# Performance work log

Measured on AMD Instinct MI355X. Metric: run time of the kernel, lower is better.

Reference implementation:

```python
import jax, jax.numpy as jnp
import numpy as np

EPS = 1e-5
K = 20
NH = 16
SLOPE = 0.2

def leaky(x):
    return jnp.where(x >= 0, x, SLOPE * x)

def bn(x, g, b, axes):
    # training-mode batch norm (biased variance), channel axis = 1
    m = x.mean(axes, keepdims=True)
    v = x.var(axes, keepdims=True)
    shp = [1] * x.ndim
    shp[1] = -1
    return (x - m) / jnp.sqrt(v + EPS) * g.reshape(shp) + b.reshape(shp)

def efr(x, idx, w, k):
    # x: [B, C, N]; idx: flat global gather indices [B*N*k]; w: [C_out, 2C+1]
    B, C, N = x.shape
    xt = x.transpose(0, 2, 1).reshape(B * N, C)
    feature = xt[idx].reshape(B, N, k, C)            # gathered neighbors
    xc = xt.reshape(B, N, 1, C)
    fmean = feature.mean(-1, keepdims=True)          # [B,N,k,1]
    f = jnp.concatenate([feature - xc, fmean, jnp.broadcast_to(xc, feature.shape)], axis=3)
    return jnp.einsum('bnkc,oc->bonk', f, w)         # 1x1 conv -> [B,C_out,N,k]


def setup_inputs() -> dict:
    key = jax.random.key(0)
    ks = jax.random.split(key, 24)
    B, N = 8, 4096
    IN_CH, FEAT_CH, OUT_CH = 6, 64, 64
    d = {}
    d['points'] = jax.random.normal(ks[0], (B, IN_CH // 2, N), dtype=jnp.float32)
    d['feat'] = jax.random.normal(ks[1], (B, FEAT_CH // 2, N), dtype=jnp.float32)
    d['idx'] = jax.random.randint(ks[2], (B * N * K,), 0, B * N)
    s = 0.1
    d['w_efr_p'] = jax.random.normal(ks[3], (IN_CH, IN_CH + 1), dtype=jnp.float32) * s
    d['w_efr_f'] = jax.random.normal(ks[4], (FEAT_CH, FEAT_CH + 1), dtype=jnp.float32) * s
    d['w_q'] = jax.random.normal(ks[5], (FEAT_CH, FEAT_CH // 2), dtype=jnp.float32) * s
    d['g_q'] = jnp.ones((FEAT_CH,), jnp.float32)
    d['b_q'] = jnp.zeros((FEAT_CH,), jnp.float32)
    d['w_pos1'] = jax.random.normal(ks[6], (IN_CH, IN_CH // 2), dtype=jnp.float32) * s
    d['g_pos1'] = jnp.ones((IN_CH,), jnp.float32)
    d['b_pos1'] = jnp.zeros((IN_CH,), jnp.float32)
    d['w_pos2'] = jax.random.normal(ks[7], (FEAT_CH, IN_CH), dtype=jnp.float32) * s
    d['w_attn'] = jax.random.normal(ks[8], (NH * IN_CH, FEAT_CH), dtype=jnp.float32) * s
    d['g1'] = jnp.ones((NH,), jnp.float32)
    d['b1'] = jnp.zeros((NH,), jnp.float32)
    d['w_lin'] = jax.random.normal(ks[9], (OUT_CH, NH), dtype=jnp.float32) * s
    d['g_lin'] = jnp.ones((OUT_CH,), jnp.float32)
    d['b_lin'] = jnp.zeros((OUT_CH,), jnp.float32)
    d['w_res'] = jax.random.normal(ks[10], (OUT_CH, FEAT_CH), dtype=jnp.float32) * s
    d['g_res'] = jnp.ones((OUT_CH,), jnp.float32)
    d['b_res'] = jnp.zeros((OUT_CH,), jnp.float32)
    return d


def reference(points, feat, idx, w_efr_p, w_efr_f, w_q, g_q, b_q,
              w_pos1, g_pos1, b_pos1, w_pos2, w_attn, g1, b1,
              w_lin, g_lin, b_lin, w_res, g_res, b_res):
    B, _, N = points.shape
    knn_points = efr(points, idx, w_efr_p, K)   # [B,6,N,K]
    knn_feat = efr(feat, idx, w_efr_f, K)       # [B,64,N,K]
    x_q = leaky(bn(jnp.einsum('bcn,oc->bon', feat, w_q), g_q, b_q, (0, 2)))
    pos = leaky(bn(jnp.einsum('bcn,oc->bon', points, w_pos1), g_pos1, b_pos1, (0, 2)))
    pos = pos[:, :, :, None] - knn_points       # [B,6,N,K]
    pos = jnp.einsum('bcnk,oc->bonk', pos, w_pos2)  # [B,64,N,K]
    attn = x_q[:, :, :, None] - knn_feat + pos
    attn = jax.nn.softmax(attn / float(np.sqrt(knn_feat.shape[1])), axis=-1)
    attn = jnp.einsum('bcnk,oc->bonk', attn, w_attn)  # [B,NH*6,N,K]
    attn5 = attn.transpose(0, 2, 3, 1).reshape(B, N, K, NH, -1)  # [B,N,K,NH,6]
    y = jnp.einsum('bnkhc,bcnk->bhnk', attn5, knn_points)        # [B,NH,N,K]
    y = leaky(bn(y, g1, b1, (0, 2, 3)))
    y = bn(jnp.einsum('bcnk,oc->bonk', y, w_lin), g_lin, b_lin, (0, 2, 3))
    res = bn(jnp.einsum('bcnk,oc->bonk', knn_feat, w_res), g_res, b_res, (0, 2, 3))
    y = leaky(y + res)
    return y.max(axis=-1)                        # [B,64,N]
```

## Files before the change

kernel.cpp:

```cpp
#include <hip/hip_runtime.h>

#define KNN 20
#define NN 4096
#define NPTS 32768
#define PPW 8

using short8 = __attribute__((ext_vector_type(8))) short;
using f32x4v = __attribute__((ext_vector_type(4))) float;
using uint4v = __attribute__((ext_vector_type(4))) unsigned int;

__device__ __forceinline__ float lrelu(float x){ return x >= 0.f ? x : 0.2f*x; }
__device__ __forceinline__ unsigned short f2b(float x){
    union { float f; unsigned u; } v; v.f = x;
    unsigned r = v.u + 0x7FFFu + ((v.u >> 16) & 1u);
    return (unsigned short)(r >> 16);
}
__device__ __forceinline__ float b2f(unsigned h){
    union { unsigned u; float f; } v; v.u = h << 16; return v.f;
}
#define WSYNC() do { asm volatile("s_waitcnt lgkmcnt(0)" ::: "memory"); __builtin_amdgcn_sched_barrier(0); } while(0)

__device__ __forceinline__ int fslot(int fragi, int klocal, int gp){
    return fragi*1024 + (((klocal) + ((gp)<<4)) ^ ((gp)*5))*16;
}

__global__ void kprep(const float* __restrict__ weff, const float* __restrict__ wattn,
                      const float* __restrict__ wres, const float* __restrict__ wl,
                      unsigned short* __restrict__ packW, float* __restrict__ wdiff,
                      float* __restrict__ w32t, float* __restrict__ wrb,
                      float* __restrict__ rww)
{
    __shared__ float sres[4096];
    __shared__ float sweff[4160];
    __shared__ float scomb[2048];
    int t = threadIdx.x;
    for (int m=t; m<4096; m+=256) sres[m] = wres[m];
    for (int m=t; m<4160; m+=256) sweff[m] = weff[m];
    __syncthreads();
    for (int q=t;q<2048;q+=256){
        int c=q>>5, j=q&31;
        wdiff[q] = sweff[c*65+33+j]-sweff[c*65+j];
    }
    if (t<64) w32t[t] = sweff[t*65+32];
    for (int q=t;q<2048;q+=256){
        int o=q>>5, j=q&31;
        float a=0.f, b=0.f;
        for (int c=0;c<64;c++){
            float wr = sres[o*64+c];
            a += wr*sweff[c*65+j];
            b += wr*(sweff[c*65+33+j]-sweff[c*65+j]);
        }
        scomb[q]=a; wrb[q]=b;
    }
    if (t<64){
        float a=0.f;
        for (int c=0;c<64;c++) a += sres[t*64+c]*sweff[c*65+32];
        rww[t]=a;
    }
    __syncthreads();
    for (int q = t; q < 1536; q += 256){
        int f = q >> 6, l = q & 63;
        #pragma unroll
        for (int j=0;j<8;j++){
            int koff, n; float v;
            if (f < 4){ n = f*16 + (l&15); koff = 0;
                int k = koff + (j>=4?16:0) + 4*(l>>4) + (j&3);
                v = sweff[n*65 + k];
            } else if (f < 16){ int ff=f-4; n = (ff>>1)*16 + (l&15); koff = (ff&1)*32;
                int k = koff + (j>=4?16:0) + 4*(l>>4) + (j&3);
                v = wattn[n*64 + k];
            } else { int ff=f-16; n = (ff>>1)*16 + (l&15); koff = (ff&1)*32;
                int k = koff + (j>=4?16:0) + 4*(l>>4) + (j&3);
                v = sres[n*64 + k];
            }
            packW[(size_t)(f*64+l)*8 + j] = f2b(v);
        }
    }
    for (int q=t;q<512;q+=256){
        int f=q>>6, l=q&63;
        int nt = f&3; bool iswl = f>=4;
        #pragma unroll
        for (int j=0;j<8;j++){
            int kdim = (j>=4?16:0)+4*(l>>4)+(j&3);
            float v;
            if (!iswl) v = scomb[(nt*16+(l&15))*32 + kdim];
            else v = (kdim<16) ? wl[(nt*16+(l&15))*16 + kdim] : 0.f;
            packW[(size_t)((24+f)*64+l)*8+j] = f2b(v);
        }
    }
}

__global__ void __launch_bounds__(256) k0_prep(
    const float* __restrict__ pts, const float* __restrict__ feat,
    const float* __restrict__ wq, const float* __restrict__ wpos1,
    const float* __restrict__ wefp, const float* __restrict__ wdiff,
    const float* __restrict__ wrb,
    unsigned short* __restrict__ ft16, float* __restrict__ pt4,
    unsigned short* __restrict__ qp16, float* __restrict__ pp,
    unsigned short* __restrict__ base16, float* __restrict__ bpp,
    unsigned short* __restrict__ rb16,
    float* __restrict__ qsum, float* __restrict__ qsq,
    float* __restrict__ psum, float* __restrict__ psq)
{
    __shared__ float swq[2048];
    __shared__ float swd[2048];
    __shared__ float swr[2048];
    __shared__ float red[4][64], red2[4][64];
    int tid = threadIdx.x;
    for (int m=tid;m<2048;m+=256){ swq[m]=wq[m]; swd[m]=wdiff[m]; swr[m]=wrb[m]; }
    __syncthreads();
    int r = blockIdx.x*256 + tid;
    int b = r >> 12, n = r & 4095;
    float p0 = pts[((size_t)b*3+0)*NN+n];
    float p1 = pts[((size_t)b*3+1)*NN+n];
    float p2 = pts[((size_t)b*3+2)*NN+n];
    float pm = (p0+p1+p2)*(1.f/3.f);
    *(float4*)(pt4 + (size_t)r*4) = make_float4(p0,p1,p2,pm);
    float f[32];
    #pragma unroll
    for (int c=0;c<32;c++) f[c] = feat[((size_t)b*32+c)*NN+n];
    #pragma unroll
    for (int c=0;c<32;c+=2){
        unsigned pk = (unsigned)f2b(f[c]) | ((unsigned)f2b(f[c+1])<<16);
        *(unsigned*)(ft16 + (size_t)r*32 + c) = pk;
    }
    float q[64];
    for (int o=0;o<64;o++){
        float a=0.f;
        #pragma unroll
        for (int c=0;c<32;c++) a += swq[o*32+c]*f[c];
        q[o]=a;
    }
    for (int o=0;o<64;o+=2){
        unsigned pk = (unsigned)f2b(q[o]) | ((unsigned)f2b(q[o+1])<<16);
        *(unsigned*)(qp16 + (size_t)r*64 + o) = pk;
    }
    int lane = tid & 63, wvv = tid>>6;
    for (int o=0;o<64;o++){
        float s=q[o], s2=q[o]*q[o];
        for (int d=1; d<64; d<<=1){ s += __shfl_xor(s,d); s2 += __shfl_xor(s2,d); }
        if (lane==0){ red[wvv][o]=s; red2[wvv][o]=s2; }
    }
    __syncthreads();
    if (tid<64){
        atomicAdd(qsum+tid, red[0][tid]+red[1][tid]+red[2][tid]+red[3][tid]);
        atomicAdd(qsq+tid, red2[0][tid]+red2[1][tid]+red2[2][tid]+red2[3][tid]);
    }
    for (int o=0;o<64;o++){
        float a=0.f;
        #pragma unroll
        for (int c=0;c<32;c++) a += swd[o*32+c]*f[c];
        q[o]=a;
    }
    for (int o=0;o<64;o+=2){
        unsigned pk = (unsigned)f2b(q[o]) | ((unsigned)f2b(q[o+1])<<16);
        *(unsigned*)(base16 + (size_t)r*64 + o) = pk;
    }
    for (int o=0;o<64;o++){
        float a=0.f;
        #pragma unroll
        for (int c=0;c<32;c++) a += swr[o*32+c]*f[c];
        q[o]=a;
    }
    for (int o=0;o<64;o+=2){
        unsigned pk = (unsigned)f2b(q[o]) | ((unsigned)f2b(q[o+1])<<16);
        *(unsigned*)(rb16 + (size_t)r*64 + o) = pk;
    }
    float pr[8];
    #pragma unroll
    for (int o=0;o<6;o++) pr[o] = wpos1[o*3]*p0 + wpos1[o*3+1]*p1 + wpos1[o*3+2]*p2;
    pr[6]=0.f; pr[7]=0.f;
    *(float4*)(pp+(size_t)r*8)   = make_float4(pr[0],pr[1],pr[2],pr[3]);
    *(float4*)(pp+(size_t)r*8+4) = make_float4(pr[4],pr[5],pr[6],pr[7]);
    __syncthreads();
    for (int o=0;o<6;o++){
        float s=pr[o], s2=pr[o]*pr[o];
        for (int d=1;d<64;d<<=1){ s += __shfl_xor(s,d); s2 += __shfl_xor(s2,d); }
        if (lane==0){ red[wvv][o]=s; red2[wvv][o]=s2; }
    }
    __syncthreads();
    if (tid<6){
        atomicAdd(psum+tid, red[0][tid]+red[1][tid]+red[2][tid]+red[3][tid]);
        atomicAdd(psq+tid, red2[0][tid]+red2[1][tid]+red2[2][tid]+red2[3][tid]);
    }
    #pragma unroll
    for (int j=0;j<6;j++)
        bpp[(size_t)r*8+j] = p0*(wefp[j*7+4]-wefp[j*7]) + p1*(wefp[j*7+5]-wefp[j*7+1])
                           + p2*(wefp[j*7+6]-wefp[j*7+2]);
    bpp[(size_t)r*8+6]=0.f; bpp[(size_t)r*8+7]=0.f;
}

__global__ void k1_paramsA(
    const float* __restrict__ qsum, const float* __restrict__ qsq,
    const float* __restrict__ psum, const float* __restrict__ psq,
    const float* __restrict__ gq, const float* __restrict__ bq,
    const float* __restrict__ gp, const float* __restrict__ bp,
    float* __restrict__ bnq_a, float* __restrict__ bnq_c,
    float* __restrict__ bnp_a, float* __restrict__ bnp_c)
{
    int t = threadIdx.x;
    const float inv = 1.f/32768.f;
    if (t < 64){
        float m = qsum[t]*inv; float v = qsq[t]*inv - m*m;
        float a = gq[t]*rsqrtf(v + 1e-5f);
        bnq_a[t] = a; bnq_c[t] = bq[t] - m*a;
    }
    if (t < 6){
        float m = psum[t]*inv; float v = psq[t]*inv - m*m;
        float a = gp[t]*rsqrtf(v + 1e-5f);
        bnp_a[t] = a; bnp_c[t] = bp[t] - m*a;
    }
}

#define ARENA 12544
#define ANB   0
#define ATR   2048
#define KFR   6272
#define SFM   10368
#define SSKP  10496
#define SIDX  11136
#define YST   11776

__global__ void __launch_bounds__(256, 3) k2_main(
    const unsigned short* __restrict__ ft16, const float* __restrict__ pt4,
    const unsigned short* __restrict__ qp16, const float* __restrict__ pp,
    const unsigned short* __restrict__ base16, const float* __restrict__ bpp,
    const int* __restrict__ idx,
    const float* __restrict__ wefp, const float* __restrict__ wpos2,
    const unsigned short* __restrict__ packW, const float* __restrict__ w32t,
    const float* __restrict__ bnq_a, const float* __restrict__ bnq_c,
    const float* __restrict__ bnp_a, const float* __restrict__ bnp_c,
    unsigned short* __restrict__ yv,
    float* __restrict__ yslot, float* __restrict__ rslot)
{
    __shared__ __align__(16) char smem_[4*ARENA];
    const int tid = threadIdx.x;
    const int l = tid & 63, wv = tid >> 6;
    const int lo = l & 15, g = l >> 4;
    char* S = smem_ + wv*ARENA;
    const int srd = (l ^ (g*5))*16;

    float w2r[4][6], w32r[4], bnqa[4], bnqc[4];
    #pragma unroll
    for (int nt=0;nt<4;nt++){
        #pragma unroll
        for (int j=0;j<6;j++) w2r[nt][j] = wpos2[(nt*16+lo)*6+j];
        w32r[nt] = w32t[nt*16+lo];
        bnqa[nt] = bnq_a[nt*16+lo];
        bnqc[nt] = bnq_c[nt*16+lo];
    }
    float bnpa[6], bnpc[6];
    #pragma unroll
    for (int j=0;j<6;j++){ bnpa[j]=bnp_a[j]; bnpc[j]=bnp_c[j]; }

    float ysum=0.f, ysq=0.f;
    float racc[4]={0.f,0.f,0.f,0.f}, rsqa[4]={0.f,0.f,0.f,0.f};

    const int rbase = blockIdx.x*(4*PPW) + wv*PPW;

    *(int*)(S+SIDX+l*4)        = idx[(size_t)rbase*KNN + l];
    *(int*)(S+SIDX+(64+l)*4)   = idx[(size_t)rbase*KNN + 64 + l];
    if (l < 32) *(int*)(S+SIDX+(128+l)*4) = idx[(size_t)rbase*KNN + 128 + l];
    WSYNC();

    uint2 ng0, ng1; uint2 ng2 = make_uint2(0u,0u); float4 ngp4 = make_float4(0,0,0,0);
    unsigned short nqr[4], nbr[4];
    float nppr[6], nbppr[6];
    float xqv[4], basev[4], sp[6];

#define ISSUE(pi_) { \
    int sb = (pi_)*KNN*4; size_t rr = (size_t)(rbase + (pi_)); \
    int i0 = *(const int*)(S+SIDX+sb+(l>>3)*4); \
    int i1 = *(const int*)(S+SIDX+sb+(8+(l>>3))*4); \
    ng0 = *(const uint2*)(ft16 + (size_t)i0*32 + (l&7)*4); \
    ng1 = *(const uint2*)(ft16 + (size_t)i1*32 + (l&7)*4); \
    if (l < 32){ int i2 = *(const int*)(S+SIDX+sb+(16+(l>>3))*4); \
                 ng2 = *(const uint2*)(ft16 + (size_t)i2*32 + (l&7)*4); } \
    if (l < KNN){ int ip = *(const int*)(S+SIDX+sb+l*4); \
                  ngp4 = *(const float4*)(pt4 + (size_t)ip*4); } \
    _Pragma("unroll") for (int nt=0;nt<4;nt++){ \
        nqr[nt] = qp16[rr*64 + nt*16+lo]; nbr[nt] = base16[rr*64 + nt*16+lo]; } \
    _Pragma("unroll") for (int j=0;j<6;j++){ nppr[j] = pp[rr*8+j]; nbppr[j] = bpp[rr*8+j]; } \
    __builtin_amdgcn_sched_barrier(0); \
}

#define STAGE() { \
    float s0 = b2f(ng0.x&0xffffu)+b2f(ng0.x>>16)+b2f(ng0.y&0xffffu)+b2f(ng0.y>>16); \
    float s1 = b2f(ng1.x&0xffffu)+b2f(ng1.x>>16)+b2f(ng1.y&0xffffu)+b2f(ng1.y>>16); \
    float s2 = b2f(ng2.x&0xffffu)+b2f(ng2.x>>16)+b2f(ng2.y&0xffffu)+b2f(ng2.y>>16); \
    s0 += __shfl_xor(s0,1); s0 += __shfl_xor(s0,2); s0 += __shfl_xor(s0,4); \
    s1 += __shfl_xor(s1,1); s1 += __shfl_xor(s1,2); s1 += __shfl_xor(s1,4); \
    s2 += __shfl_xor(s2,1); s2 += __shfl_xor(s2,2); s2 += __shfl_xor(s2,4); \
    if ((l&7)==0){ \
        *(float*)(S+SFM+(l>>3)*4) = s0*(1.f/32.f); \
        *(float*)(S+SFM+(8+(l>>3))*4) = s1*(1.f/32.f); \
        if (l < 32) *(float*)(S+SFM+(16+(l>>3))*4) = s2*(1.f/32.f); \
    } \
    { int kk = l>>3, gp_ = l&3, jb = ((l>>2)&1)*8; \
      *(uint2*)(S + ANB + fslot(0, kk, gp_) + jb) = ng0; \
      *(uint2*)(S + ANB + fslot(0, 8+kk, gp_) + jb) = ng1; \
      if (l < 32) *(uint2*)(S + ANB + fslot(1, kk, gp_) + jb) = ng2; } \
    if (l < KNN){ \
        _Pragma("unroll") for (int j=0;j<6;j++){ \
            float v = nbppr[j] + wefp[j*7]*ngp4.x + wefp[j*7+1]*ngp4.y \
                    + wefp[j*7+2]*ngp4.z + wefp[j*7+3]*ngp4.w; \
            *(float*)(S+SSKP+(l*8+j)*4) = v; } } \
    _Pragma("unroll") for (int nt=0;nt<4;nt++){ \
        xqv[nt] = lrelu(bnqa[nt]*b2f(nqr[nt]) + bnqc[nt]); \
        basev[nt] = b2f(nbr[nt]); } \
    _Pragma("unroll") for (int j=0;j<6;j++) sp[j] = lrelu(bnpa[j]*nppr[j] + bnpc[j]); \
    WSYNC(); \
}

    ISSUE(0);
    STAGE();

    for (int pi=0; pi<PPW; pi++){
        const size_t r = (size_t)(rbase + pi);
        if (pi < PPW-1) ISSUE(pi+1);

        f32x4v C1[2][4];
        #pragma unroll
        for (int mt=0;mt<2;mt++)
            #pragma unroll
            for (int nt=0;nt<4;nt++)
                #pragma unroll
                for (int i=0;i<4;i++) C1[mt][nt][i] = 0.f;
        short8 Af0 = *(const short8*)(S + ANB + 0*1024 + srd);
        short8 Af1 = *(const short8*)(S + ANB + 1*1024 + srd);
        #pragma unroll
        for (int nt=0;nt<4;nt++){
            short8 Bf = *(const short8*)(packW + (size_t)(nt*64 + l)*8);
            C1[0][nt] = __builtin_amdgcn_mfma_f32_16x16x32_bf16(Af0, Bf, C1[0][nt], 0, 0, 0);
            C1[1][nt] = __builtin_amdgcn_mfma_f32_16x16x32_bf16(Af1, Bf, C1[1][nt], 0, 0, 0);
        }
        #pragma unroll
        for (int mt=0;mt<2;mt++){
            #pragma unroll
            for (int i=0;i<4;i++){
                int k = mt*16 + g*4 + i;
                bool valid = (k < KNN);
                int kk = valid ? k : 0;
                float fmk = *(const float*)(S+SFM+kk*4);
                float sk[6];
                #pragma unroll
                for (int j=0;j<6;j++) sk[j] = *(const float*)(S+SSKP+(kk*8+j)*4);
                #pragma unroll
                for (int nt=0;nt<4;nt++){
                    float kf = C1[mt][nt][i] + basev[nt] + w32r[nt]*fmk;
                    if (valid){
                        int fa = fslot(mt*2+(nt>>1), g*4+i, lo>>2) + ((nt&1)*4 + (lo&3))*2;
                        *(unsigned short*)(S + KFR + fa) = f2b(kf);
                    }
                    float pos = 0.f;
                    #pragma unroll
                    for (int j=0;j<6;j++) pos += (sp[j]-sk[j])*w2r[nt][j];
                    C1[mt][nt][i] = valid ? (xqv[nt] - kf + pos)*0.125f : -1e30f;
                }
            }
        }
        #pragma unroll
        for (int nt=0;nt<4;nt++){
            float mx = -1e30f;
            #pragma unroll
            for (int mt=0;mt<2;mt++)
                #pragma unroll
                for (int i=0;i<4;i++) mx = fmaxf(mx, C1[mt][nt][i]);
            mx = fmaxf(mx, __shfl_xor(mx,16));
            mx = fmaxf(mx, __shfl_xor(mx,32));
            float sm = 0.f;
            #pragma unroll
            for (int mt=0;mt<2;mt++)
                #pragma unroll
                for (int i=0;i<4;i++){ float e = __expf(C1[mt][nt][i]-mx); C1[mt][nt][i]=e; sm += e; }
            sm += __shfl_xor(sm,16);
            sm += __shfl_xor(sm,32);
            float inv = 1.f/sm;
            #pragma unroll
            for (int mt=0;mt<2;mt++)
                #pragma unroll
                for (int i=0;i<4;i++){
                    int k = mt*16 + g*4 + i;
                    if (k < KNN){
                        int fa = fslot(mt*2+(nt>>1), g*4+i, lo>>2) + ((nt&1)*4 + (lo&3))*2;
                        *(unsigned short*)(S + ATR + fa) = f2b(C1[mt][nt][i]*inv);
                    }
                }
        }
        WSYNC();
        short8 Aa[2][2];
        #pragma unroll
        for (int mt=0;mt<2;mt++)
            #pragma unroll
            for (int s=0;s<2;s++) Aa[mt][s] = *(const short8*)(S + ATR + (mt*2+s)*1024 + srd);
        f32x4v C2[2][6];
        #pragma unroll
        for (int mt=0;mt<2;mt++)
            #pragma unroll
            for (int nt=0;nt<6;nt++)
                #pragma unroll
                for (int i=0;i<4;i++) C2[mt][nt][i] = 0.f;
        #pragma unroll
        for (int nt=0;nt<6;nt++){
            #pragma unroll
            for (int s=0;s<2;s++){
                short8 Bf = *(const short8*)(packW + (size_t)((4+nt*2+s)*64 + l)*8);
                #pragma unroll
                for (int mt=0;mt<2;mt++)
                    C2[mt][nt] = __builtin_amdgcn_mfma_f32_16x16x32_bf16(Aa[mt][s], Bf, C2[mt][nt], 0, 0, 0);
            }
        }
        WSYNC();
        #pragma unroll
        for (int mt=0;mt<2;mt++)
            #pragma unroll
            for (int nt=0;nt<6;nt++)
                #pragma unroll
                for (int i=0;i<4;i++){
                    int k = mt*16 + g*4 + i;
                    if (k < KNN)
                        *(unsigned short*)(S + ATR + k*208 + (nt*16+lo)*2) = f2b(C2[mt][nt][i]);
                }
        WSYNC();
        #pragma unroll
        for (int it=0; it<5; it++){
            int kq = it*4 + g;
            const char* row = S + ATR + kq*208 + lo*12;
            unsigned d0 = *(const unsigned*)(row);
            unsigned d1 = *(const unsigned*)(row+4);
            unsigned d2 = *(const unsigned*)(row+8);
            float yval = b2f(d0&0xffffu) * (*(const float*)(S+SSKP+(kq*8+0)*4))
                       + b2f(d0>>16)    * (*(const float*)(S+SSKP+(kq*8+1)*4))
                       + b2f(d1&0xffffu)* (*(const float*)(S+SSKP+(kq*8+2)*4))
                       + b2f(d1>>16)    * (*(const float*)(S+SSKP+(kq*8+3)*4))
                       + b2f(d2&0xffffu)* (*(const float*)(S+SSKP+(kq*8+4)*4))
                       + b2f(d2>>16)    * (*(const float*)(S+SSKP+(kq*8+5)*4));
            *(unsigned short*)(S + YST + kq*32 + lo*2) = f2b(yval);
            ysum += yval; ysq += yval*yval;
        }
        short8 Ak[2][2];
        #pragma unroll
        for (int mt=0;mt<2;mt++)
            #pragma unroll
            for (int s=0;s<2;s++) Ak[mt][s] = *(const short8*)(S + KFR + (mt*2+s)*1024 + srd);
        f32x4v C3[2][4];
        #pragma unroll
        for (int mt=0;mt<2;mt++)
            #pragma unroll
            for (int nt=0;nt<4;nt++)
                #pragma unroll
                for (int i=0;i<4;i++) C3[mt][nt][i] = 0.f;
        #pragma unroll
        for (int nt=0;nt<4;nt++){
            #pragma unroll
            for (int s=0;s<2;s++){
                short8 Bf = *(const short8*)(packW + (size_t)((16+nt*2+s)*64 + l)*8);
                #pragma unroll
                for (int mt=0;mt<2;mt++)
                    C3[mt][nt] = __builtin_amdgcn_mfma_f32_16x16x32_bf16(Ak[mt][s], Bf, C3[mt][nt], 0, 0, 0);
            }
        }
        #pragma unroll
        for (int mt=0;mt<2;mt++)
            #pragma unroll
            for (int i=0;i<4;i++){
                int k = mt*16 + g*4 + i;
                if (k < KNN){
                    #pragma unroll
                    for (int nt=0;nt<4;nt++){
                        float v = C3[mt][nt][i];
                        racc[nt] += v; rsqa[nt] += v*v;
                    }
                }
            }
        WSYNC();
        if (l < 40){
            uint4v v = *(const uint4v*)(S + YST + l*16);
            *(uint4v*)((char*)yv + r*640 + l*16) = v;
        }
        if (pi < PPW-1) STAGE();
    }
    ysum += __shfl_xor(ysum,16); ysum += __shfl_xor(ysum,32);
    ysq  += __shfl_xor(ysq,16);  ysq  += __shfl_xor(ysq,32);
    #pragma unroll
    for (int nt=0;nt<4;nt++){
        racc[nt] += __shfl_xor(racc[nt],16); racc[nt] += __shfl_xor(racc[nt],32);
        rsqa[nt] += __shfl_xor(rsqa[nt],16); rsqa[nt] += __shfl_xor(rsqa[nt],32);
    }
    int slot = (blockIdx.x*4 + wv) & 63;
    if (l < 16){
        atomicAdd(yslot + slot*32 + l, ysum);
        #pragma unroll
        for (int nt=0;nt<4;nt++) atomicAdd(rslot + slot*128 + nt*16 + l, racc[nt]);
    } else if (l < 32){
        atomicAdd(yslot + slot*32 + 16 + lo, ysq);
        #pragma unroll
        for (int nt=0;nt<4;nt++) atomicAdd(rslot + slot*128 + 64 + nt*16 + lo, rsqa[nt]);
    }
#undef ISSUE
#undef STAGE
}

__global__ void k3_paramsB(
    const float* __restrict__ yslot, const float* __restrict__ rslot,
    const float* __restrict__ g1, const float* __restrict__ b1,
    const float* __restrict__ gr, const float* __restrict__ br,
    float* __restrict__ bn1_a, float* __restrict__ bn1_c,
    float* __restrict__ bnr_a, float* __restrict__ bnr_c)
{
    __shared__ float sy[32];
    __shared__ float sr[128];
    int t = threadIdx.x;
    float s1 = 0.f;
    if (t < 32){ for (int i=0;i<64;i++) s1 += yslot[(size_t)i*32+t]; }
    float s2 = 0.f;
    for (int i=0;i<64;i++) s2 += rslot[(size_t)i*128+t];
    if (t < 32) sy[t] = s1;
    sr[t] = s2;
    __syncthreads();
    const float inv = 1.f/655360.f;
    if (t < 16){
        float m = sy[t]*inv; float v = sy[16+t]*inv - m*m;
        float a = g1[t]*rsqrtf(v + 1e-5f);
        bn1_a[t] = a; bn1_c[t] = b1[t] - m*a;
    }
    if (t < 64){
        float m = sr[t]*inv; float v = sr[64+t]*inv - m*m;
        float a = gr[t]*rsqrtf(v + 1e-5f);
        bnr_a[t] = a; bnr_c[t] = br[t] - m*a;
    }
}

__global__ void __launch_bounds__(256) k4_linstats(
    const unsigned short* __restrict__ yv,
    const float* __restrict__ bn1_a, const float* __restrict__ bn1_c,
    float* __restrict__ Mslot, float* __restrict__ Sslot)
{
    __shared__ __align__(16) char lds[4*1024];
    const int tid = threadIdx.x, l = tid & 63, wvv = tid >> 6;
    const int lo = l & 15, g = l >> 4;
    char* L = lds + wvv*1024;
    const int h0 = (l&1)*8;
    float a8[8], c8[8];
    #pragma unroll
    for (int j=0;j<8;j++){ a8[j]=bn1_a[h0+j]; c8[j]=bn1_c[h0+j]; }
    short8 ones;
    #pragma unroll
    for (int j=0;j<8;j++) ones[j] = (short)0x3F80;
    f32x4v Macc, Sacc;
    #pragma unroll
    for (int i=0;i<4;i++){ Macc[i]=0.f; Sacc[i]=0.f; }
    const int waveid = blockIdx.x*4 + wvv;
    for (int it=0; it<5; it++){
        size_t s0 = ((size_t)waveid*5 + it)*32;
        uint4 v = *(const uint4*)(yv + s0*16 + l*8);
        unsigned short e0 = v.x&0xffffu, e1 = v.x>>16, e2 = v.y&0xffffu, e3 = v.y>>16;
        unsigned short e4 = v.z&0xffffu, e5 = v.z>>16, e6 = v.w&0xffffu, e7 = v.w>>16;
        float y0 = lrelu(a8[0]*b2f(e0)+c8[0]), y1 = lrelu(a8[1]*b2f(e1)+c8[1]);
        float y2_ = lrelu(a8[2]*b2f(e2)+c8[2]), y3 = lrelu(a8[3]*b2f(e3)+c8[3]);
        float y4 = lrelu(a8[4]*b2f(e4)+c8[4]), y5 = lrelu(a8[5]*b2f(e5)+c8[5]);
        float y6 = lrelu(a8[6]*b2f(e6)+c8[6]), y7 = lrelu(a8[7]*b2f(e7)+c8[7]);
        uint4 o;
        o.x = (unsigned)f2b(y0) | ((unsigned)f2b(y1)<<16);
        o.y = (unsigned)f2b(y2_)| ((unsigned)f2b(y3)<<16);
        o.z = (unsigned)f2b(y4) | ((unsigned)f2b(y5)<<16);
        o.w = (unsigned)f2b(y6) | ((unsigned)f2b(y7)<<16);
        *(uint4*)(L + l*16) = o;
        WSYNC();
        short8 Af;
        #pragma unroll
        for (int j=0;j<8;j++){
            int s = 4*g + (j&3) + ((j>=4)?16:0);
            Af[j] = *(const short*)(L + s*32 + lo*2);
        }
        WSYNC();
        Macc = __builtin_amdgcn_mfma_f32_16x16x32_bf16(Af, Af, Macc, 0, 0, 0);
        Sacc = __builtin_amdgcn_mfma_f32_16x16x32_bf16(ones, Af, Sacc, 0, 0, 0);
    }
    float* Ms = Mslot + (size_t)(waveid&15)*256;
    #pragma unroll
    for (int i=0;i<4;i++) atomicAdd(Ms + (g*4+i)*16 + lo, Macc[i]);
    if (l < 16) atomicAdd(Sslot + (size_t)(waveid&15)*16 + lo, Sacc[0]);
}

__global__ void k5_paramsC(
    const float* __restrict__ Mslot, const float* __restrict__ Sslot,
    const float* __restrict__ wl,
    const float* __restrict__ gl, const float* __restrict__ bl,
    float* __restrict__ bnl_a, float* __restrict__ bnl_c)
{
    __shared__ float Ms[256], Ss[16];
    int t = threadIdx.x;
    float m = 0.f;
    for (int i=0;i<16;i++) m += Mslot[(size_t)i*256+t];
    Ms[t] = m;
    if (t < 16){
        float s = 0.f;
        for (int i=0;i<16;i++) s += Sslot[(size_t)i*16+t];
        Ss[t] = s;
    }
    __syncthreads();
    if (t < 64){
        float w[16];
        #pragma unroll
        for (int h=0;h<16;h++) w[h] = wl[t*16+h];
        float lsum = 0.f;
        #pragma unroll
        for (int h=0;h<16;h++) lsum += w[h]*Ss[h];
        float lsq = 0.f;
        for (int h1=0;h1<16;h1++){
            float acc = 0.f;
            #pragma unroll
            for (int h2=0;h2<16;h2++) acc += Ms[h1*16+h2]*w[h2];
            lsq += w[h1]*acc;
        }
        const float inv = 1.f/655360.f;
        float mean = lsum*inv; float var = lsq*inv - mean*mean;
        float a = gl[t]*rsqrtf(var + 1e-5f);
        bnl_a[t] = a; bnl_c[t] = bl[t] - mean*a;
    }
}

#define ARENA6 2848
#define SFM6 2048
#define SIDX6 2176

__global__ void __launch_bounds__(256) k6_final(
    const unsigned short* __restrict__ ft16, const unsigned short* __restrict__ yv,
    const int* __restrict__ idx, const unsigned short* __restrict__ rb16,
    const unsigned short* __restrict__ packW, const float* __restrict__ rww,
    const float* __restrict__ bn1_a, const float* __restrict__ bn1_c,
    const float* __restrict__ bnl_a, const float* __restrict__ bnl_c,
    const float* __restrict__ bnr_a, const float* __restrict__ bnr_c,
    float* __restrict__ out)
{
    __shared__ __align__(16) char smem_[4*ARENA6];
    __shared__ float sval[64*36];
    const int tid = threadIdx.x;
    const int l = tid & 63, wv = tid >> 6;
    const int lo = l & 15, g = l >> 4;
    char* S = smem_ + wv*ARENA6;
    const int srd = (l ^ (g*5))*16;

    short8 Bc[4], Bl[4];
    #pragma unroll
    for (int nt=0;nt<4;nt++){
        Bc[nt] = *(const short8*)(packW + (size_t)((24+nt)*64+l)*8);
        Bl[nt] = *(const short8*)(packW + (size_t)((28+nt)*64+l)*8);
    }
    float4 b1a = *(const float4*)(bn1_a + 4*g);
    float4 b1c = *(const float4*)(bn1_c + 4*g);
    float la[4], lc[4], ra[4], rc[4], rwv[4];
    #pragma unroll
    for (int nt=0;nt<4;nt++){
        int o = nt*16+lo;
        la[nt]=bnl_a[o]; lc[nt]=bnl_c[o]; ra[nt]=bnr_a[o]; rc[nt]=bnr_c[o]; rwv[nt]=rww[o];
    }
    const int rbase = blockIdx.x*32 + wv*8;
    *(int*)(S+SIDX6+l*4)      = idx[(size_t)rbase*KNN + l];
    *(int*)(S+SIDX6+(64+l)*4) = idx[(size_t)rbase*KNN + 64 + l];
    if (l < 32) *(int*)(S+SIDX6+(128+l)*4) = idx[(size_t)rbase*KNN + 128 + l];
    WSYNC();

    uint2 ng0, ng1; uint2 ng2 = make_uint2(0u,0u);
    uint2 ylo_, yhi_; unsigned short rbr[4];
    short8 AlyA, AlyB; float rbv[4];

#define ISSUE6(pi_) { \
    int sb = (pi_)*KNN*4; size_t rr = (size_t)(rbase + (pi_)); \
    int i0 = *(const int*)(S+SIDX6+sb+(l>>3)*4); \
    int i1 = *(const int*)(S+SIDX6+sb+(8+(l>>3))*4); \
    ng0 = *(const uint2*)(ft16 + (size_t)i0*32 + (l&7)*4); \
    ng1 = *(const uint2*)(ft16 + (size_t)i1*32 + (l&7)*4); \
    if (l < 32){ int i2 = *(const int*)(S+SIDX6+sb+(16+(l>>3))*4); \
                 ng2 = *(const uint2*)(ft16 + (size_t)i2*32 + (l&7)*4); } \
    ylo_ = *(const uint2*)(yv + rr*320 + (l&15)*16 + g*4); \
    yhi_ = make_uint2(0u,0u); \
    if (lo < 4) yhi_ = *(const uint2*)(yv + rr*320 + (16+(l&15))*16 + g*4); \
    _Pragma("unroll") for (int nt=0;nt<4;nt++) rbr[nt] = rb16[rr*64 + nt*16+lo]; \
    __builtin_amdgcn_sched_barrier(0); \
}

#define STAGE6() { \
    float s0 = b2f(ng0.x&0xffffu)+b2f(ng0.x>>16)+b2f(ng0.y&0xffffu)+b2f(ng0.y>>16); \
    float s1 = b2f(ng1.x&0xffffu)+b2f(ng1.x>>16)+b2f(ng1.y&0xffffu)+b2f(ng1.y>>16); \
    float s2 = b2f(ng2.x&0xffffu)+b2f(ng2.x>>16)+b2f(ng2.y&0xffffu)+b2f(ng2.y>>16); \
    s0 += __shfl_xor(s0,1); s0 += __shfl_xor(s0,2); s0 += __shfl_xor(s0,4); \
    s1 += __shfl_xor(s1,1); s1 += __shfl_xor(s1,2); s1 += __shfl_xor(s1,4); \
    s2 += __shfl_xor(s2,1); s2 += __shfl_xor(s2,2); s2 += __shfl_xor(s2,4); \
    if ((l&7)==0){ \
        *(float*)(S+SFM6+(l>>3)*4) = s0*(1.f/32.f); \
        *(float*)(S+SFM6+(8+(l>>3))*4) = s1*(1.f/32.f); \
        if (l < 32) *(float*)(S+SFM6+(16+(l>>3))*4) = s2*(1.f/32.f); \
    } \
    { int kk = l>>3, gp_ = l&3, jb = ((l>>2)&1)*8; \
      *(uint2*)(S + fslot(0, kk, gp_) + jb) = ng0; \
      *(uint2*)(S + fslot(0, 8+kk, gp_) + jb) = ng1; \
      if (l < 32) *(uint2*)(S + fslot(1, kk, gp_) + jb) = ng2; } \
    { float t0 = lrelu(b1a.x*b2f(ylo_.x&0xffffu)+b1c.x); \
      float t1 = lrelu(b1a.y*b2f(ylo_.x>>16)+b1c.y); \
      float t2 = lrelu(b1a.z*b2f(ylo_.y&0xffffu)+b1c.z); \
      float t3 = lrelu(b1a.w*b2f(ylo_.y>>16)+b1c.w); \
      AlyA[0]=(short)f2b(t0); AlyA[1]=(short)f2b(t1); AlyA[2]=(short)f2b(t2); AlyA[3]=(short)f2b(t3); \
      AlyA[4]=0; AlyA[5]=0; AlyA[6]=0; AlyA[7]=0; \
      t0 = lrelu(b1a.x*b2f(yhi_.x&0xffffu)+b1c.x); \
      t1 = lrelu(b1a.y*b2f(yhi_.x>>16)+b1c.y); \
      t2 = lrelu(b1a.z*b2f(yhi_.y&0xffffu)+b1c.z); \
      t3 = lrelu(b1a.w*b2f(yhi_.y>>16)+b1c.w); \
      AlyB[0]=(short)f2b(t0); AlyB[1]=(short)f2b(t1); AlyB[2]=(short)f2b(t2); AlyB[3]=(short)f2b(t3); \
      AlyB[4]=0; AlyB[5]=0; AlyB[6]=0; AlyB[7]=0; } \
    _Pragma("unroll") for (int nt=0;nt<4;nt++) rbv[nt] = b2f(rbr[nt]); \
    WSYNC(); \
}

    ISSUE6(0);
    STAGE6();

    for (int pi=0; pi<8; pi++){
        if (pi < 7) ISSUE6(pi+1);
        short8 Af0 = *(const short8*)(S + 0*1024 + srd);
        short8 Af1 = *(const short8*)(S + 1*1024 + srd);
        f32x4v Crv[2][4], Clv[2][4];
        #pragma unroll
        for (int mt=0;mt<2;mt++)
            #pragma unroll
            for (int nt=0;nt<4;nt++)
                #pragma unroll
                for (int i=0;i<4;i++){ Crv[mt][nt][i]=0.f; Clv[mt][nt][i]=0.f; }
        #pragma unroll
        for (int nt=0;nt<4;nt++){
            Crv[0][nt] = __builtin_amdgcn_mfma_f32_16x16x32_bf16(Af0, Bc[nt], Crv[0][nt], 0, 0, 0);
            Crv[1][nt] = __builtin_amdgcn_mfma_f32_16x16x32_bf16(Af1, Bc[nt], Crv[1][nt], 0, 0, 0);
            Clv[0][nt] = __builtin_amdgcn_mfma_f32_16x16x32_bf16(AlyA, Bl[nt], Clv[0][nt], 0, 0, 0);
            Clv[1][nt] = __builtin_amdgcn_mfma_f32_16x16x32_bf16(AlyB, Bl[nt], Clv[1][nt], 0, 0, 0);
        }
        float vmax[4] = {-1e30f,-1e30f,-1e30f,-1e30f};
        #pragma unroll
        for (int mt=0;mt<2;mt++)
            #pragma unroll
            for (int i=0;i<4;i++){
                int k = mt*16 + g*4 + i;
                if (k < KNN){
                    float fmk = *(const float*)(S+SFM6+k*4);
                    #pragma unroll
                    for (int nt=0;nt<4;nt++){
                        float rv = Crv[mt][nt][i] + rbv[nt] + rwv[nt]*fmk;
                        float lv = Clv[mt][nt][i];
                        float val = lrelu(la[nt]*lv + lc[nt] + ra[nt]*rv + rc[nt]);
                        vmax[nt] = fmaxf(vmax[nt], val);
                    }
                }
            }
        #pragma unroll
        for (int nt=0;nt<4;nt++){
            vmax[nt] = fmaxf(vmax[nt], __shfl_xor(vmax[nt],16));
            vmax[nt] = fmaxf(vmax[nt], __shfl_xor(vmax[nt],32));
        }
        if (l < 16){
            #pragma unroll
            for (int nt=0;nt<4;nt++)
                sval[(nt*16+lo)*36 + wv*8 + pi] = vmax[nt];
        }
        if (pi < 7) STAGE6();
    }
    __syncthreads();
    {
        int o = tid >> 2, seg = tid & 3;
        float4 v0 = *(const float4*)(sval + o*36 + seg*8);
        float4 v1 = *(const float4*)(sval + o*36 + seg*8 + 4);
        size_t base = ((size_t)(blockIdx.x>>7)*64 + o)*NN + (blockIdx.x&127)*32 + seg*8;
        *(float4*)(out + base) = v0;
        *(float4*)(out + base + 4) = v1;
    }
#undef ISSUE6
#undef STAGE6
}

extern "C" void kernel_launch(void* const* d_in, const int* in_sizes, int n_in,
                              void* d_out, int out_size, void* d_ws, size_t ws_size,
                              hipStream_t stream)
{
    const float* pts   = (const float*)d_in[0];
    const float* feat  = (const float*)d_in[1];
    const int*   idx   = (const int*)d_in[2];
    const float* wefp  = (const float*)d_in[3];
    const float* weff  = (const float*)d_in[4];
    const float* wq    = (const float*)d_in[5];
    const float* gq    = (const float*)d_in[6];
    const float* bq    = (const float*)d_in[7];
    const float* wpos1 = (const float*)d_in[8];
    const float* gp    = (const float*)d_in[9];
    const float* bp    = (const float*)d_in[10];
    const float* wpos2 = (const float*)d_in[11];
    const float* wattn = (const float*)d_in[12];
    const float* g1    = (const float*)d_in[13];
    const float* b1    = (const float*)d_in[14];
    const float* wl    = (const float*)d_in[15];
    const float* gl    = (const float*)d_in[16];
    const float* bl    = (const float*)d_in[17];
    const float* wres  = (const float*)d_in[18];
    const float* gr    = (const float*)d_in[19];
    const float* br    = (const float*)d_in[20];
    float* out = (float*)d_out;

    char* ws = (char*)d_ws;
    size_t o_ft16 = 0;
    size_t o_pt4  = o_ft16 + (size_t)NPTS*64;
    size_t o_qp16 = o_pt4  + (size_t)NPTS*16;
    size_t o_pp   = o_qp16 + (size_t)NPTS*128;
    size_t o_b16  = o_pp   + (size_t)NPTS*32;
    size_t o_bpp  = o_b16  + (size_t)NPTS*128;
    size_t o_rb16 = o_bpp  + (size_t)NPTS*32;
    size_t o_packW= o_rb16 + (size_t)NPTS*128;
    size_t o_wdiff= o_packW + 32*512*2;
    size_t o_wrb  = o_wdiff + 2048*4;
    size_t o_rw   = o_wrb   + 2048*4;
    size_t o_w32  = o_rw    + 64*4;
    size_t o_st   = o_w32   + 64*4;
    size_t o_qsum  = o_st;
    size_t o_qsq   = o_qsum + 64*4;
    size_t o_psum  = o_qsq  + 64*4;
    size_t o_psq   = o_psum + 8*4;
    size_t o_yslot = o_psq  + 8*4;
    size_t o_rslot = o_yslot + (size_t)64*32*4;
    size_t o_mslot = o_rslot + (size_t)64*128*4;
    size_t o_sslot = o_mslot + (size_t)16*256*4;
    size_t zero_bytes = (o_sslot + (size_t)16*16*4) - o_st;
    size_t o_par   = o_st + zero_bytes;
    size_t o_bnq_a = o_par;
    size_t o_bnq_c = o_bnq_a + 64*4;
    size_t o_bnp_a = o_bnq_c + 64*4;
    size_t o_bnp_c = o_bnp_a + 8*4;
    size_t o_bn1_a = o_bnp_c + 8*4;
    size_t o_bn1_c = o_bn1_a + 16*4;
    size_t o_bnl_a = o_bn1_c + 16*4;
    size_t o_bnl_c = o_bnl_a + 64*4;
    size_t o_bnr_a = o_bnl_c + 64*4;
    size_t o_bnr_c = o_bnr_a + 64*4;
    size_t o_yv = (o_bnr_c + 64*4 + 255) & ~(size_t)255;

    unsigned short* ft16 = (unsigned short*)(ws + o_ft16);
    float* pt4  = (float*)(ws + o_pt4);
    unsigned short* qp16 = (unsigned short*)(ws + o_qp16);
    float* ppb  = (float*)(ws + o_pp);
    unsigned short* b16p = (unsigned short*)(ws + o_b16);
    float* bppb = (float*)(ws + o_bpp);
    unsigned short* rb16 = (unsigned short*)(ws + o_rb16);
    unsigned short* packW = (unsigned short*)(ws + o_packW);
    float* wdiff= (float*)(ws + o_wdiff);
    float* wrb  = (float*)(ws + o_wrb);
    float* rww  = (float*)(ws + o_rw);
    float* w32t = (float*)(ws + o_w32);
    float* qsum = (float*)(ws + o_qsum);
    float* qsq  = (float*)(ws + o_qsq);
    float* psum = (float*)(ws + o_psum);
    float* psq  = (float*)(ws + o_psq);
    float* yslot= (float*)(ws + o_yslot);
    float* rslot= (float*)(ws + o_rslot);
    float* Mslot= (float*)(ws + o_mslot);
    float* Sslot= (float*)(ws + o_sslot);
    float* bnq_a= (float*)(ws + o_bnq_a);
    float* bnq_c= (float*)(ws + o_bnq_c);
    float* bnp_a= (float*)(ws + o_bnp_a);
    float* bnp_c= (float*)(ws + o_bnp_c);
    float* bn1_a= (float*)(ws + o_bn1_a);
    float* bn1_c= (float*)(ws + o_bn1_c);
    float* bnl_a= (float*)(ws + o_bnl_a);
    float* bnl_c= (float*)(ws + o_bnl_c);
    float* bnr_a= (float*)(ws + o_bnr_a);
    float* bnr_c= (float*)(ws + o_bnr_c);
    unsigned short* yvp = (unsigned short*)(ws + o_yv);

    (void)hipMemsetAsync(ws + o_st, 0, zero_bytes, stream);

    kprep<<<1, 256, 0, stream>>>(weff, wattn, wres, wl, packW, wdiff, w32t, wrb, rww);
    k0_prep<<<128, 256, 0, stream>>>(pts, feat, wq, wpos1, wefp, wdiff, wrb,
                                     ft16, pt4, qp16, ppb, b16p, bppb, rb16,
                                     qsum, qsq, psum, psq);
    k1_paramsA<<<1, 64, 0, stream>>>(qsum, qsq, psum, psq, gq, bq, gp, bp,
                                     bnq_a, bnq_c, bnp_a, bnp_c);
    k2_main<<<NPTS/(4*PPW), 256, 0, stream>>>(ft16, pt4, qp16, ppb, b16p, bppb, idx,
                                     wefp, wpos2, packW, w32t,
                                     bnq_a, bnq_c, bnp_a, bnp_c,
                                     yvp, yslot, rslot);
    k3_paramsB<<<1, 128, 0, stream>>>(yslot, rslot, g1, b1, gr, br,
                                      bn1_a, bn1_c, bnr_a, bnr_c);
    k4_linstats<<<1024, 256, 0, stream>>>(yvp, bn1_a, bn1_c, Mslot, Sslot);
    k5_paramsC<<<1, 256, 0, stream>>>(Mslot, Sslot, wl, gl, bl, bnl_a, bnl_c);
    k6_final<<<1024, 256, 0, stream>>>(ft16, yvp, idx, rb16, packW, rww,
                                       bn1_a, bn1_c, bnl_a, bnl_c, bnr_a, bnr_c, out);
}
```

Measured before the change: 562.7 us.

## Shrink per-wave LDS arena by aliasing buffers and raise occupancy to 4

Reorders the per-point pipeline so the residual MFMA (C3) runs right after the softmax, with its key-feature fragments read together with the attention fragments. This frees the gathered-neighbour and key-feature regions for reuse as attention and C2 staging. The LDS arena per wave drops from 12544 to 10240 bytes and launch bounds go from 3 to 4 blocks per CU, to add occupancy and latency hiding. In exchange, more accumulators are live at the same time (C3 alongside C2), which raises register pressure under a tighter register cap and may cause spills.

```diff
diff --git a/kernel.cpp b/kernel.cpp
--- a/kernel.cpp
+++ b/kernel.cpp
@@ -212,16 +212,15 @@
     }
 }
 
-#define ARENA 12544
-#define ANB   0
-#define ATR   2048
-#define KFR   6272
-#define SFM   10368
-#define SSKP  10496
-#define SIDX  11136
-#define YST   11776
-
-__global__ void __launch_bounds__(256, 3) k2_main(
+#define ARENA 10240
+#define R1    0
+#define R2    4096
+#define SFM   8192
+#define SSKP  8320
+#define SIDX  8960
+#define YST   9600
+
+__global__ void __launch_bounds__(256, 4) k2_main(
     const unsigned short* __restrict__ ft16, const float* __restrict__ pt4,
     const unsigned short* __restrict__ qp16, const float* __restrict__ pp,
     const unsigned short* __restrict__ base16, const float* __restrict__ bpp,
@@ -297,9 +296,9 @@
         if (l < 32) *(float*)(S+SFM+(16+(l>>3))*4) = s2*(1.f/32.f); \
     } \
     { int kk = l>>3, gp_ = l&3, jb = ((l>>2)&1)*8; \
-      *(uint2*)(S + ANB + fslot(0, kk, gp_) + jb) = ng0; \
-      *(uint2*)(S + ANB + fslot(0, 8+kk, gp_) + jb) = ng1; \
-      if (l < 32) *(uint2*)(S + ANB + fslot(1, kk, gp_) + jb) = ng2; } \
+      *(uint2*)(S + R1 + fslot(0, kk, gp_) + jb) = ng0; \
+      *(uint2*)(S + R1 + fslot(0, 8+kk, gp_) + jb) = ng1; \
+      if (l < 32) *(uint2*)(S + R1 + fslot(1, kk, gp_) + jb) = ng2; } \
     if (l < KNN){ \
         _Pragma("unroll") for (int j=0;j<6;j++){ \
             float v = nbppr[j] + wefp[j*7]*ngp4.x + wefp[j*7+1]*ngp4.y \
@@ -326,8 +325,8 @@
             for (int nt=0;nt<4;nt++)
                 #pragma unroll
                 for (int i=0;i<4;i++) C1[mt][nt][i] = 0.f;
-        short8 Af0 = *(const short8*)(S + ANB + 0*1024 + srd);
-        short8 Af1 = *(const short8*)(S + ANB + 1*1024 + srd);
+        short8 Af0 = *(const short8*)(S + R1 + 0*1024 + srd);
+        short8 Af1 = *(const short8*)(S + R1 + 1*1024 + srd);
         #pragma unroll
         for (int nt=0;nt<4;nt++){
             short8 Bf = *(const short8*)(packW + (size_t)(nt*64 + l)*8);
@@ -350,7 +349,7 @@
                     float kf = C1[mt][nt][i] + basev[nt] + w32r[nt]*fmk;
                     if (valid){
                         int fa = fslot(mt*2+(nt>>1), g*4+i, lo>>2) + ((nt&1)*4 + (lo&3))*2;
-                        *(unsigned short*)(S + KFR + fa) = f2b(kf);
+                        *(unsigned short*)(S + R2 + fa) = f2b(kf);
                     }
                     float pos = 0.f;
                     #pragma unroll
@@ -383,16 +382,36 @@
                     int k = mt*16 + g*4 + i;
                     if (k < KNN){
                         int fa = fslot(mt*2+(nt>>1), g*4+i, lo>>2) + ((nt&1)*4 + (lo&3))*2;
-                        *(unsigned short*)(S + ATR + fa) = f2b(C1[mt][nt][i]*inv);
+                        *(unsigned short*)(S + R1 + fa) = f2b(C1[mt][nt][i]*inv);
                     }
                 }
         }
         WSYNC();
-        short8 Aa[2][2];
+        short8 Ak[2][2], Aa[2][2];
         #pragma unroll
         for (int mt=0;mt<2;mt++)
             #pragma unroll
-            for (int s=0;s<2;s++) Aa[mt][s] = *(const short8*)(S + ATR + (mt*2+s)*1024 + srd);
+            for (int s=0;s<2;s++){
+                Ak[mt][s] = *(const short8*)(S + R2 + (mt*2+s)*1024 + srd);
+                Aa[mt][s] = *(const short8*)(S + R1 + (mt*2+s)*1024 + srd);
+            }
+        f32x4v C3[2][4];
+        #pragma unroll
+        for (int mt=0;mt<2;mt++)
+            #pragma unroll
+            for (int nt=0;nt<4;nt++)
+                #pragma unroll
+                for (int i=0;i<4;i++) C3[mt][nt][i] = 0.f;
+        #pragma unroll
+        for (int nt=0;nt<4;nt++){
+            #pragma unroll
+            for (int s=0;s<2;s++){
+                short8 Bf = *(const short8*)(packW + (size_t)((16+nt*2+s)*64 + l)*8);
+                #pragma unroll
+                for (int mt=0;mt<2;mt++)
+                    C3[mt][nt] = __builtin_amdgcn_mfma_f32_16x16x32_bf16(Ak[mt][s], Bf, C3[mt][nt], 0, 0, 0);
+            }
+        }
         f32x4v C2[2][6];
         #pragma unroll
         for (int mt=0;mt<2;mt++)
@@ -410,7 +429,19 @@
                     C2[mt][nt] = __builtin_amdgcn_mfma_f32_16x16x32_bf16(Aa[mt][s], Bf, C2[mt][nt], 0, 0, 0);
             }
         }
-        WSYNC();
+        #pragma unroll
+        for (int mt=0;mt<2;mt++)
+            #pragma unroll
+            for (int i=0;i<4;i++){
+                int k = mt*16 + g*4 + i;
+                if (k < KNN){
+                    #pragma unroll
+                    for (int nt=0;nt<4;nt++){
+                        float v = C3[mt][nt][i];
+                        racc[nt] += v; rsqa[nt] += v*v;
+                    }
+                }
+            }
         #pragma unroll
         for (int mt=0;mt<2;mt++)
             #pragma unroll
@@ -419,13 +450,13 @@
                 for (int i=0;i<4;i++){
                     int k = mt*16 + g*4 + i;
                     if (k < KNN)
-                        *(unsigned short*)(S + ATR + k*208 + (nt*16+lo)*2) = f2b(C2[mt][nt][i]);
+                        *(unsigned short*)(S + R2 + k*200 + (nt*16+lo)*2) = f2b(C2[mt][nt][i]);
                 }
         WSYNC();
         #pragma unroll
         for (int it=0; it<5; it++){
             int kq = it*4 + g;
-            const char* row = S + ATR + kq*208 + lo*12;
+            const char* row = S + R2 + kq*200 + lo*12;
             unsigned d0 = *(const unsigned*)(row);
             unsigned d1 = *(const unsigned*)(row+4);
             unsigned d2 = *(const unsigned*)(row+8);
@@ -438,41 +469,6 @@
             *(unsigned short*)(S + YST + kq*32 + lo*2) = f2b(yval);
             ysum += yval; ysq += yval*yval;
         }
-        short8 Ak[2][2];
-        #pragma unroll
-        for (int mt=0;mt<2;mt++)
-            #pragma unroll
-            for (int s=0;s<2;s++) Ak[mt][s] = *(const short8*)(S + KFR + (mt*2+s)*1024 + srd);
-        f32x4v C3[2][4];
-        #pragma unroll
-        for (int mt=0;mt<2;mt++)
-            #pragma unroll
-            for (int nt=0;nt<4;nt++)
-                #pragma unroll
-                for (int i=0;i<4;i++) C3[mt][nt][i] = 0.f;
-        #pragma unroll
-        for (int nt=0;nt<4;nt++){
-            #pragma unroll
-            for (int s=0;s<2;s++){
-                short8 Bf = *(const short8*)(packW + (size_t)((16+nt*2+s)*64 + l)*8);
-                #pragma unroll
-                for (int mt=0;mt<2;mt++)
-                    C3[mt][nt] = __builtin_amdgcn_mfma_f32_16x16x32_bf16(Ak[mt][s], Bf, C3[mt][nt], 0, 0, 0);
-            }
-        }
-        #pragma unroll
-        for (int mt=0;mt<2;mt++)
-            #pragma unroll
-            for (int i=0;i<4;i++){
-                int k = mt*16 + g*4 + i;
-                if (k < KNN){
-                    #pragma unroll
-                    for (int nt=0;nt<4;nt++){
-                        float v = C3[mt][nt][i];
-                        racc[nt] += v; rsqa[nt] += v*v;
-                    }
-                }
-            }
         WSYNC();
         if (l < 40){
             uint4v v = *(const uint4v*)(S + YST + l*16);
```

Result: slower. 644.2 us (+14.5%).
